# Kernel optimization log

Hardware: AMD Instinct MI355X
Metric: run time of the kernel (lower is better)

Reference implementation:

```python
import jax, jax.numpy as jnp
import numpy as np

EPS = 1e-5
NUM_HEADS = 8


def _conv(x, w, pad, dil=1, groups=1, b=None):
    y = jax.lax.conv_general_dilated(
        x, w, (1, 1), pad, rhs_dilation=(dil, dil),
        dimension_numbers=('NCHW', 'OIHW', 'NCHW'), feature_group_count=groups)
    if b is not None:
        y = y + b[None, :, None, None]
    return y


def _bn_relu(x, gamma, beta):
    # BatchNorm2d in training mode: batch statistics over (N,H,W) per channel
    mu = x.mean(axis=(0, 2, 3), keepdims=True)
    var = x.var(axis=(0, 2, 3), keepdims=True)
    y = (x - mu) / jnp.sqrt(var + EPS) * gamma[None, :, None, None] + beta[None, :, None, None]
    return jax.nn.relu(y)


def _ln(x, w, b):
    # WithBias LayerNorm over channel dim (to_3d makes C the last axis)
    mu = x.mean(axis=1, keepdims=True)
    var = x.var(axis=1, keepdims=True)
    return (x - mu) / jnp.sqrt(var + EPS) * w[None, :, None, None] + b[None, :, None, None]


def _l2n(t):
    # torch F.normalize: x / max(||x||_2, 1e-12)
    return t / jnp.maximum(jnp.linalg.norm(t, axis=-1, keepdims=True), 1e-12)


def _forward(x, ln_w, ln_b, wd1, gd1, bd1, wd2, gd2, bd2, wd3, gd3, bd3,
             w_out1, w1, b1, w2, b2, w3, b3, w4, b4, w5, b5, w6, b6, w_out2):
    B, C, H, W = x.shape
    head, ch = NUM_HEADS, C // NUM_HEADS
    x1 = _ln(x, ln_w, ln_b)
    # dilated dense-conv branch (DConv2d = conv -> BN -> ReLU), dilations [1,6,12]
    x11 = _bn_relu(_conv(x, wd1, ((0, 0), (0, 0))), gd1, bd1)
    x12 = _bn_relu(_conv(x, wd2, ((6, 6), (6, 6)), dil=6), gd2, bd2)
    x13 = _bn_relu(_conv(x, wd3, ((12, 12), (12, 12)), dil=12), gd3, bd3)
    out2 = _conv(x11 + x12 + x13, w_out1, ((0, 0), (0, 0))) + x
    # six depthwise conv branches, summed
    att = (_conv(x1, w1, ((0, 0), (2, 2)), groups=C, b=b1)
           + _conv(x1, w2, ((2, 2), (0, 0)), groups=C, b=b2)
           + _conv(x1, w3, ((0, 0), (0, 0)), groups=C, b=b3)
           + _conv(x1, w4, ((1, 1), (1, 1)), groups=C, b=b4)
           + _conv(x1, w5, ((0, 0), (3, 3)), groups=C, b=b5)
           + _conv(x1, w6, ((3, 3), (0, 0)), groups=C, b=b6))
    out1 = _conv(att, w_out2, ((0, 0), (0, 0)))

    def r_hwc(t):  # b (head c) h w -> b head h (w c)
        return t.reshape(B, head, ch, H, W).transpose(0, 1, 3, 4, 2).reshape(B, head, H, W * ch)

    def r_whc(t):  # b (head c) h w -> b head w (h c)
        return t.reshape(B, head, ch, H, W).transpose(0, 1, 4, 3, 2).reshape(B, head, W, H * ch)

    k1 = _l2n(r_hwc(out1))
    v1 = r_hwc(out1)
    k2 = _l2n(r_whc(out2))
    v2 = r_whc(out2)
    q2 = _l2n(r_whc(out1))
    q1 = _l2n(r_whc(out2))
    A1 = jax.nn.softmax(q1 @ jnp.swapaxes(k1, -2, -1), axis=-1)  # [B,head,W,H]
    out3 = A1 @ v1 + q1
    A2 = jax.nn.softmax(q2 @ jnp.swapaxes(k2, -2, -1), axis=-1)
    out4 = A2 @ v2 + q2
    # b head h (w c) -> b (head c) h w
    o3 = out3.reshape(B, head, H, W, ch).transpose(0, 1, 4, 2, 3).reshape(B, C, H, W)
    # b head w (h c) -> b (head c) h w
    o4 = out4.reshape(B, head, W, H, ch).transpose(0, 1, 4, 3, 2).reshape(B, C, H, W)
    return _conv(o3, w_out2, ((0, 0), (0, 0))) + _conv(o4, w_out2, ((0, 0), (0, 0))) + x


def setup_inputs() -> dict:
    key = jax.random.key(0)
    ks = jax.random.split(key, 16)
    B, C, H, W = 8, 128, 128, 128

    def rn(k, shape, s):
        return jax.random.normal(k, shape, jnp.float32) * s

    inp = {}
    inp['x'] = jax.random.normal(ks[0], (B, C, H, W), jnp.float32)
    inp['ln_w'] = jnp.ones((C,), jnp.float32)
    inp['ln_b'] = jnp.zeros((C,), jnp.float32)
    inp['wd1'] = rn(ks[1], (C, C, 1, 1), 0.1)
    inp['gd1'] = jnp.ones((C,), jnp.float32)
    inp['bd1'] = jnp.zeros((C,), jnp.float32)
    inp['wd2'] = rn(ks[2], (C, C, 3, 3), 0.04)
    inp['gd2'] = jnp.ones((C,), jnp.float32)
    inp['bd2'] = jnp.zeros((C,), jnp.float32)
    inp['wd3'] = rn(ks[3], (C, C, 3, 3), 0.04)
    inp['gd3'] = jnp.ones((C,), jnp.float32)
    inp['bd3'] = jnp.zeros((C,), jnp.float32)
    inp['w_out1'] = rn(ks[4], (C, C, 1, 1), 0.09)
    inp['w1'] = rn(ks[5], (C, 1, 1, 5), 0.3)
    inp['b1'] = jnp.zeros((C,), jnp.float32)
    inp['w2'] = rn(ks[6], (C, 1, 5, 1), 0.3)
    inp['b2'] = jnp.zeros((C,), jnp.float32)
    inp['w3'] = rn(ks[7], (C, 1, 1, 1), 0.5)
    inp['b3'] = jnp.zeros((C,), jnp.float32)
    inp['w4'] = rn(ks[8], (C, 1, 3, 3), 0.2)
    inp['b4'] = jnp.zeros((C,), jnp.float32)
    inp['w5'] = rn(ks[9], (C, 1, 1, 7), 0.25)
    inp['b5'] = jnp.zeros((C,), jnp.float32)
    inp['w6'] = rn(ks[10], (C, 1, 7, 1), 0.25)
    inp['b6'] = jnp.zeros((C,), jnp.float32)
    inp['w_out2'] = rn(ks[11], (C, C, 1, 1), 0.09)
    return inp


def reference(x, ln_w, ln_b, wd1, gd1, bd1, wd2, gd2, bd2, wd3, gd3, bd3,
              w_out1, w1, b1, w2, b2, w3, b3, w4, b4, w5, b5, w6, b6, w_out2):
    return _forward(x, ln_w, ln_b, wd1, gd1, bd1, wd2, gd2, bd2, wd3, gd3, bd3,
                    w_out1, w1, b1, w2, b2, w3, b3, w4, b4, w5, b5, w6, b6, w_out2)
```

## Files before the change

### kernel.cpp

```cpp
#include <hip/hip_runtime.h>

#define Bb 8
#define Cc 128
#define Hh 128
#define Ww 128
#define HW 16384
#define CHW (Cc*HW)
#define NHW (Bb*HW)
#define CH 16
#define EPS 1e-5f

typedef __attribute__((ext_vector_type(8))) short bf16x8;
typedef __attribute__((ext_vector_type(4))) float f32x4;

static __device__ __forceinline__ short f2b(float f) {
  unsigned u = __float_as_uint(f);
  unsigned lsb = (u >> 16) & 1;
  return (short)((u + 0x7fffu + lsb) >> 16);
}
static __device__ __forceinline__ float b2f(short s) {
  return __uint_as_float(((unsigned)(unsigned short)s) << 16);
}

__global__ __launch_bounds__(256) void k_ln(const float* __restrict__ x,
    const float* __restrict__ g, const float* __restrict__ be,
    float* __restrict__ y)
{
  int p = blockIdx.x*256 + threadIdx.x;
  int b = p >> 14, hw = p & 16383;
  const float* xp = x + (long)b*CHW + hw;
  float s = 0.f, q = 0.f;
  for (int c = 0; c < Cc; ++c) { float v = xp[c*HW]; s += v; q += v*v; }
  float mu = s * (1.f/Cc);
  float var = q * (1.f/Cc) - mu*mu;
  float rstd = rsqrtf(var + EPS);
  float* yp = y + (long)b*CHW + hw;
  for (int c = 0; c < Cc; ++c) {
    float v = xp[c*HW];
    yp[c*HW] = (v - mu) * rstd * g[c] + be[c];
  }
}

__global__ __launch_bounds__(256) void k_reorg3b(const float* __restrict__ Wt, short* __restrict__ out)
{
  int idx = blockIdx.x*256 + threadIdx.x;
  int tap = idx >> 14, r = idx & 16383;
  out[idx] = f2b(Wt[r*9 + tap]);
}

__global__ __launch_bounds__(256) void k_cast(const float* __restrict__ in, short* __restrict__ out)
{
  int i = blockIdx.x*256 + threadIdx.x;
  out[i] = f2b(in[i]);
}

__global__ __launch_bounds__(256) void k_zero(float* p, int n)
{
  int i = blockIdx.x*256 + threadIdx.x;
  if (i < n) p[i] = 0.f;
}

__global__ __launch_bounds__(256) void k_nhwc(const float* __restrict__ in, short* __restrict__ out)
{
  __shared__ float Ls[32][33];
  int bid = blockIdx.x;
  int hwt = bid & 511, c4 = (bid>>9)&3, b = bid>>11;
  int hw0 = hwt << 5, c0 = c4 << 5;
  int t = threadIdx.x;
  int hl = t & 31, cl = t >> 5;
  const float* p = in + (long)b*CHW + hw0;
  for (int r = cl; r < 32; r += 8)
    Ls[r][hl] = p[(long)(c0+r)*HW + hl];
  __syncthreads();
  short* q = out + ((long)b*HW + hw0)*Cc + c0;
  int ccl = t & 31, hl0 = t >> 5;
  for (int r = hl0; r < 32; r += 8)
    q[(long)r*Cc + ccl] = f2b(Ls[ccl][r]);
}

__global__ __launch_bounds__(256,2) void k_mconv(const short* __restrict__ X,
    const short* __restrict__ W, const float* __restrict__ res,
    float* __restrict__ Y, int k3, int dil)
{
  __shared__ short Ws[128*136];
  __shared__ short Xs[152*136];
  int b = blockIdx.x >> 7, h = blockIdx.x & 127;
  int t = threadIdx.x;
  int wave = t >> 6, lane = t & 63;
  int co0 = (wave >> 1) << 6, sp0 = (wave & 1) << 6;
  int lm = lane & 15, quad = lane >> 4;
  f32x4 acc[4][4];
  #pragma unroll
  for (int i = 0; i < 4; ++i)
    #pragma unroll
    for (int j = 0; j < 4; ++j) acc[i][j] = (f32x4){0.f,0.f,0.f,0.f};
  int half = k3 >> 1;

  {
    f32x4 z = {0.f,0.f,0.f,0.f};
    for (int i = t; i < 408; i += 256) {
      int r = i / 17, o = i - r*17;
      int row = r < 12 ? r : r + 128;
      *(f32x4*)(Xs + row*136 + o*8) = z;
    }
  }

  for (int kh = 0; kh < k3; ++kh) {
    int hs = h + (kh - half)*dil;
    if ((unsigned)hs >= (unsigned)Hh) continue;
    __syncthreads();
    {
      const short* xr = X + ((long)(b*Hh + hs)*Ww)*Cc;
      #pragma unroll
      for (int it = 0; it < 8; ++it) {
        int i = t + it*256;
        int row = i >> 4, off = (i & 15) << 3;
        *(f32x4*)(Xs + (12 + row)*136 + off) = *(const f32x4*)(xr + (long)row*Cc + off);
      }
    }
    for (int kw = 0; kw < k3; ++kw) {
      int dw = (kw - half)*dil;
      if (kw) __syncthreads();
      {
        const short* wt = W + (kh*k3 + kw)*16384;
        #pragma unroll
        for (int it = 0; it < 8; ++it) {
          int i = t + it*256;
          int row = i >> 4, off = (i & 15) << 3;
          *(f32x4*)(Ws + row*136 + off) = *(const f32x4*)(wt + (long)row*128 + off);
        }
      }
      __syncthreads();
      int xrow0 = 12 + dw + sp0;
      for (int kc = 0; kc < 4; ++kc) {
        int k0 = kc << 5;
        bf16x8 af[4], bfr[4];
        #pragma unroll
        for (int i = 0; i < 4; ++i)
          af[i] = *(const bf16x8*)(Ws + (co0 + i*16 + lm)*136 + k0 + quad*8);
        #pragma unroll
        for (int j = 0; j < 4; ++j)
          bfr[j] = *(const bf16x8*)(Xs + (xrow0 + j*16 + lm)*136 + k0 + quad*8);
        #pragma unroll
        for (int i = 0; i < 4; ++i)
          #pragma unroll
          for (int j = 0; j < 4; ++j)
            acc[i][j] = __builtin_amdgcn_mfma_f32_16x16x32_bf16(af[i], bfr[j], acc[i][j], 0, 0, 0);
      }
    }
  }
  #pragma unroll
  for (int i = 0; i < 4; ++i) {
    int co = co0 + i*16 + quad*4;
    #pragma unroll
    for (int j = 0; j < 4; ++j) {
      int wc = sp0 + j*16 + lm;
      long base = ((long)(b*Cc + co)*Hh + h)*Ww + wc;
      #pragma unroll
      for (int r = 0; r < 4; ++r) {
        float v = acc[i][j][r];
        long idx = base + (long)r*HW;
        if (res) v += res[idx];
        Y[idx] = v;
      }
    }
  }
}

__global__ __launch_bounds__(256,4) void k_mconv1(const short* __restrict__ X,
    const short* __restrict__ W, const float* __restrict__ res,
    float* __restrict__ Y)
{
  __shared__ short Ws[128*136];
  int b = blockIdx.x >> 7, h = blockIdx.x & 127;
  int t = threadIdx.x;
  int wave = t >> 6, lane = t & 63;
  int co0 = (wave >> 1) << 6, sp0 = (wave & 1) << 6;
  int lm = lane & 15, quad = lane >> 4;
  #pragma unroll
  for (int it = 0; it < 8; ++it) {
    int i = t + it*256;
    int row = i >> 4, off = (i & 15) << 3;
    *(f32x4*)(Ws + row*136 + off) = *(const f32x4*)(W + (long)row*128 + off);
  }
  f32x4 acc[4][4];
  #pragma unroll
  for (int i = 0; i < 4; ++i)
    #pragma unroll
    for (int j = 0; j < 4; ++j) acc[i][j] = (f32x4){0.f,0.f,0.f,0.f};
  const short* xr = X + ((long)(b*Hh + h)*Ww)*Cc;
  __syncthreads();
  #pragma unroll
  for (int kc = 0; kc < 4; ++kc) {
    int k0 = kc << 5;
    bf16x8 af[4], bfr[4];
    #pragma unroll
    for (int j = 0; j < 4; ++j)
      bfr[j] = *(const bf16x8*)(xr + (long)(sp0 + j*16 + lm)*Cc + k0 + quad*8);
    #pragma unroll
    for (int i = 0; i < 4; ++i)
      af[i] = *(const bf16x8*)(Ws + (co0 + i*16 + lm)*136 + k0 + quad*8);
    #pragma unroll
    for (int i = 0; i < 4; ++i)
      #pragma unroll
      for (int j = 0; j < 4; ++j)
        acc[i][j] = __builtin_amdgcn_mfma_f32_16x16x32_bf16(af[i], bfr[j], acc[i][j], 0, 0, 0);
  }
  #pragma unroll
  for (int i = 0; i < 4; ++i) {
    int co = co0 + i*16 + quad*4;
    #pragma unroll
    for (int j = 0; j < 4; ++j) {
      int wc = sp0 + j*16 + lm;
      long base = ((long)(b*Cc + co)*Hh + h)*Ww + wc;
      #pragma unroll
      for (int r = 0; r < 4; ++r) {
        float v = acc[i][j][r];
        long idx = base + (long)r*HW;
        if (res) v += res[idx];
        Y[idx] = v;
      }
    }
  }
}

__global__ __launch_bounds__(256) void k_bnstats(const float* __restrict__ y1,
    const float* __restrict__ y2, const float* __restrict__ y3,
    float* __restrict__ stats)
{
  __shared__ float red[512];
  int bid = blockIdx.x;
  int tsel = bid >> 10;
  int rem = bid & 1023;
  int c = rem >> 3, b = rem & 7;
  const float* y = tsel == 0 ? y1 : (tsel == 1 ? y2 : y3);
  const float* p = y + (long)(b*Cc + c)*HW;
  float s = 0.f, q = 0.f;
  for (int i = threadIdx.x; i < HW; i += 256) { float v = p[i]; s += v; q += v*v; }
  red[threadIdx.x] = s; red[256+threadIdx.x] = q;
  __syncthreads();
  for (int st = 128; st > 0; st >>= 1) {
    if (threadIdx.x < st) {
      red[threadIdx.x] += red[threadIdx.x+st];
      red[256+threadIdx.x] += red[256+threadIdx.x+st];
    }
    __syncthreads();
  }
  if (threadIdx.x == 0) {
    atomicAdd(&stats[tsel*256 + c], red[0]);
    atomicAdd(&stats[tsel*256 + 128 + c], red[256]);
  }
}

__global__ __launch_bounds__(256) void k_bnapply(const float* y1,
    const float* __restrict__ y2, const float* __restrict__ y3,
    const float* __restrict__ stats,
    const float* __restrict__ g1, const float* __restrict__ be1,
    const float* __restrict__ g2, const float* __restrict__ be2,
    const float* __restrict__ g3, const float* __restrict__ be3,
    float* out)
{
  int i4 = blockIdx.x*256 + threadIdx.x;
  int c = (i4 >> 12) & 127;
  const float inv = 1.f/(float)NHW;
  float mu1 = stats[c]*inv;       float v1 = stats[128+c]*inv - mu1*mu1;
  float mu2 = stats[256+c]*inv;   float v2 = stats[384+c]*inv - mu2*mu2;
  float mu3 = stats[512+c]*inv;   float v3 = stats[640+c]*inv - mu3*mu3;
  float s1 = rsqrtf(v1+EPS)*g1[c], s2 = rsqrtf(v2+EPS)*g2[c], s3 = rsqrtf(v3+EPS)*g3[c];
  float o1 = be1[c]-mu1*s1, o2 = be2[c]-mu2*s2, o3_ = be3[c]-mu3*s3;
  float4 a = ((const float4*)y1)[i4];
  float4 bq = ((const float4*)y2)[i4];
  float4 cq = ((const float4*)y3)[i4];
  float4 r;
  r.x = fmaxf(fmaf(a.x,s1,o1),0.f)+fmaxf(fmaf(bq.x,s2,o2),0.f)+fmaxf(fmaf(cq.x,s3,o3_),0.f);
  r.y = fmaxf(fmaf(a.y,s1,o1),0.f)+fmaxf(fmaf(bq.y,s2,o2),0.f)+fmaxf(fmaf(cq.y,s3,o3_),0.f);
  r.z = fmaxf(fmaf(a.z,s1,o1),0.f)+fmaxf(fmaf(bq.z,s2,o2),0.f)+fmaxf(fmaf(cq.z,s3,o3_),0.f);
  r.w = fmaxf(fmaf(a.w,s1,o1),0.f)+fmaxf(fmaf(bq.w,s2,o2),0.f)+fmaxf(fmaf(cq.w,s3,o3_),0.f);
  ((float4*)out)[i4] = r;
}

__global__ __launch_bounds__(256) void k_dw2(const float* __restrict__ X,
    const float* __restrict__ w1, const float* __restrict__ b1,
    const float* __restrict__ w2, const float* __restrict__ b2,
    const float* __restrict__ w3, const float* __restrict__ b3,
    const float* __restrict__ w4, const float* __restrict__ b4,
    const float* __restrict__ w5, const float* __restrict__ b5,
    const float* __restrict__ w6, const float* __restrict__ b6,
    float* __restrict__ Y)
{
  __shared__ float Ls[38][136];
  int bid = blockIdx.x;
  int tile = bid & 3, plane = bid >> 2;
  int c = plane & 127;
  int h0 = tile << 5;
  int t = threadIdx.x;

  float hcoef[7], vcoef[7], k9[9];
  #pragma unroll
  for (int d = 0; d < 7; ++d) { hcoef[d] = w5[c*7+d]; vcoef[d] = w6[c*7+d]; }
  #pragma unroll
  for (int d = 1; d < 6; ++d) { hcoef[d] += w1[c*5+d-1]; vcoef[d] += w2[c*5+d-1]; }
  hcoef[3] += w3[c];
  #pragma unroll
  for (int k = 0; k < 9; ++k) k9[k] = w4[c*9+k];
  float bias = b1[c]+b2[c]+b3[c]+b4[c]+b5[c]+b6[c];

  const float* xp = X + (long)plane*HW;

  f32x4* lz = (f32x4*)&Ls[0][0];
  for (int i = t; i < 1292; i += 256) lz[i] = (f32x4){0.f,0.f,0.f,0.f};
  __syncthreads();
  for (int i = t; i < 1216; i += 256) {
    int r = i >> 5, cg = (i & 31) << 2;
    int h = h0 - 3 + r;
    if ((unsigned)h < 128u)
      *(f32x4*)&Ls[r][4 + cg] = *(const f32x4*)(xp + h*128 + cg);
  }
  __syncthreads();

  int g = t & 31, rs = t >> 5;
  int w0 = g << 2;
  float* Yp = Y + (long)plane*HW;

  for (int ro = 0; ro < 4; ++ro) {
    int lr = rs + (ro << 3);
    int R = lr + 3;
    f32x4 a0 = *(const f32x4*)&Ls[R][w0];
    f32x4 a1 = *(const f32x4*)&Ls[R][w0+4];
    f32x4 a2 = *(const f32x4*)&Ls[R][w0+8];
    f32x4 u0 = *(const f32x4*)&Ls[R-1][w0];
    f32x4 u1 = *(const f32x4*)&Ls[R-1][w0+4];
    f32x4 u2 = *(const f32x4*)&Ls[R-1][w0+8];
    f32x4 d0 = *(const f32x4*)&Ls[R+1][w0];
    f32x4 d1 = *(const f32x4*)&Ls[R+1][w0+4];
    f32x4 d2 = *(const f32x4*)&Ls[R+1][w0+8];
    f32x4 v3u = *(const f32x4*)&Ls[R-3][w0+4];
    f32x4 v2u = *(const f32x4*)&Ls[R-2][w0+4];
    f32x4 v2d = *(const f32x4*)&Ls[R+2][w0+4];
    f32x4 v3d = *(const f32x4*)&Ls[R+3][w0+4];

    float cr[12], ur[12], dr[12];
    #pragma unroll
    for (int k = 0; k < 4; ++k) {
      cr[k] = a0[k]; cr[4+k] = a1[k]; cr[8+k] = a2[k];
      ur[k] = u0[k]; ur[4+k] = u1[k]; ur[8+k] = u2[k];
      dr[k] = d0[k]; dr[4+k] = d1[k]; dr[8+k] = d2[k];
    }

    f32x4 o;
    #pragma unroll
    for (int j = 0; j < 4; ++j) {
      float acc = bias;
      #pragma unroll
      for (int d = 0; d < 7; ++d) acc = fmaf(hcoef[d], cr[j+d+1], acc);
      acc = fmaf(vcoef[0], v3u[j], acc);
      acc = fmaf(vcoef[1], v2u[j], acc);
      acc = fmaf(vcoef[2], ur[j+4], acc);
      acc = fmaf(vcoef[3], cr[j+4], acc);
      acc = fmaf(vcoef[4], dr[j+4], acc);
      acc = fmaf(vcoef[5], v2d[j], acc);
      acc = fmaf(vcoef[6], v3d[j], acc);
      #pragma unroll
      for (int kw = 0; kw < 3; ++kw) {
        acc = fmaf(k9[kw],   ur[j+3+kw], acc);
        acc = fmaf(k9[3+kw], cr[j+3+kw], acc);
        acc = fmaf(k9[6+kw], dr[j+3+kw], acc);
      }
      o[j] = acc;
    }
    *(f32x4*)(Yp + (h0 + lr)*128 + w0) = o;
  }
}

__global__ __launch_bounds__(256) void k_normh(const float* __restrict__ out1, float* __restrict__ invn)
{
  __shared__ float red[256];
  int bid = blockIdx.x;
  int h = bid & 127; int bh = bid >> 7;
  int b = bh >> 3, hd = bh & 7;
  const float* p = out1 + ((long)(b*Cc + hd*CH)*Hh + h)*Ww;
  float s = 0.f;
  for (int e = threadIdx.x; e < 2048; e += 256) {
    int c = e >> 7, w = e & 127;
    float v = p[(long)c*HW + w];
    s += v*v;
  }
  red[threadIdx.x] = s; __syncthreads();
  for (int st = 128; st > 0; st >>= 1) {
    if (threadIdx.x < st) red[threadIdx.x] += red[threadIdx.x+st];
    __syncthreads();
  }
  if (threadIdx.x == 0) invn[bid] = 1.f/fmaxf(sqrtf(red[0]), 1e-12f);
}

__global__ __launch_bounds__(256) void k_normw_part(const float* __restrict__ out1,
    const float* __restrict__ out2, float* __restrict__ acc1, float* __restrict__ acc2)
{
  __shared__ float red[4][256];
  int bid = blockIdx.x;
  int c = bid & 15, bh = (bid >> 4) & 63, tsel = bid >> 10;
  int b = bh >> 3, hd = bh & 7;
  const float* p = (tsel ? out2 : out1) + (long)(b*Cc + hd*CH + c)*HW;
  int t = threadIdx.x;
  const float4* p4 = (const float4*)p;
  float s0 = 0.f, s1 = 0.f, s2 = 0.f, s3 = 0.f;
  for (int i = t; i < 4096; i += 256) {
    float4 v = p4[i];
    s0 += v.x*v.x; s1 += v.y*v.y; s2 += v.z*v.z; s3 += v.w*v.w;
  }
  red[0][t] = s0; red[1][t] = s1; red[2][t] = s2; red[3][t] = s3;
  __syncthreads();
  if (t < 128) {
    int j = t >> 5;
    int g = t & 31;
    float tot = 0.f;
    #pragma unroll
    for (int r = 0; r < 8; ++r) tot += red[j][g + r*32];
    atomicAdd((tsel ? acc2 : acc1) + bh*128 + g*4 + j, tot);
  }
}

__global__ __launch_bounds__(256) void k_finw(float* __restrict__ p)
{
  int i = blockIdx.x*256 + threadIdx.x;
  float v = p[i];
  p[i] = 1.f/fmaxf(sqrtf(v), 1e-12f);
}

__global__ __launch_bounds__(256) void k_t12(const float* __restrict__ out1,
    const float* __restrict__ out2, short* __restrict__ out1T, short* __restrict__ out2T)
{
  __shared__ float Ls[32][33];
  int bid = blockIdx.x;
  int wt = bid&3, ht=(bid>>2)&3, c=(bid>>4)&127, b=(bid>>11)&7, src=bid>>14;
  const float* in = (src ? out2 : out1) + (long)(b*128+c)*16384;
  short* outp = (src ? out2T : out1T) + ((long)(b*8 + (c>>4))*128)*2048 + (c&15)*128;
  int h0 = ht*32, w0 = wt*32;
  int t = threadIdx.x, li = t&31, r0 = t>>5;
  for (int r = r0; r < 32; r += 8)
    Ls[r][li] = in[(h0+r)*128 + w0 + li];
  __syncthreads();
  for (int r = r0; r < 32; r += 8)
    outp[(long)(w0+r)*2048 + h0 + li] = f2b(Ls[li][r]);
}

__global__ __launch_bounds__(256) void k_h12(const float* __restrict__ out1,
    const float* __restrict__ out2, short* __restrict__ out1H, short* __restrict__ out2H)
{
  int bid = blockIdx.x;
  int src = bid >> 13;
  long e = ((long)(bid & 8191)*256 + threadIdx.x) * 8;
  const float* p;
  short* dst;
  if (src) { p = out2 + e; dst = out2H + e; }
  else {
    int c = (int)((e>>7)&15), h = (int)((e>>11)&127), hd=(int)((e>>18)&7), b=(int)(e>>21);
    int pp = (int)(e & 127);
    p = out1 + (((long)(b*128 + hd*16 + c)*128 + h)*128 + pp);
    dst = out1H + e;
  }
  int4 o;
  o.x = ((int)(unsigned short)f2b(p[1])<<16) | (unsigned short)f2b(p[0]);
  o.y = ((int)(unsigned short)f2b(p[3])<<16) | (unsigned short)f2b(p[2]);
  o.z = ((int)(unsigned short)f2b(p[5])<<16) | (unsigned short)f2b(p[4]);
  o.w = ((int)(unsigned short)f2b(p[7])<<16) | (unsigned short)f2b(p[6]);
  *(int4*)dst = o;
}

__global__ __launch_bounds__(256) void k_attnS_m(
    const short* __restrict__ out1T, const short* __restrict__ out2T,
    const short* __restrict__ out1H,
    const float* __restrict__ invn1h, const float* __restrict__ invn1w,
    const float* __restrict__ invn2w,
    short* __restrict__ A1b, short* __restrict__ A2b)
{
  __shared__ short As[128*72];
  __shared__ short Bs[128*72];
  int bid = blockIdx.x;
  int type = bid >> 6, bh = bid & 63;
  const short* Aop = (type ? out1T : out2T) + (long)bh*262144;
  const short* Bop = (type ? out2T : out1H) + (long)bh*262144;
  const float* invrow = (type ? invn1w : invn2w) + bh*128;
  const float* invcol = (type ? invn2w : invn1h) + bh*128;
  short* Aout = (type ? A2b : A1b) + (long)bh*16384;
  int t = threadIdx.x;
  int wave = t >> 6, lane = t & 63, lm = lane & 15, quad = lane >> 4;
  int m0 = wave << 5;
  f32x4 acc[2][8];
  #pragma unroll
  for (int i = 0; i < 2; ++i)
    #pragma unroll
    for (int j = 0; j < 8; ++j) acc[i][j] = (f32x4){0.f,0.f,0.f,0.f};
  for (int kc = 0; kc < 32; ++kc) {
    int k0 = kc << 6;
    __syncthreads();
    #pragma unroll
    for (int i = 0; i < 4; ++i) {
      int e = t + i*256;
      int row = e >> 3, off = (e & 7) << 3;
      *(float4*)(As + row*72 + off) = *(const float4*)(Aop + (long)row*2048 + k0 + off);
      *(float4*)(Bs + row*72 + off) = *(const float4*)(Bop + (long)row*2048 + k0 + off);
    }
    __syncthreads();
    #pragma unroll
    for (int ks = 0; ks < 64; ks += 32) {
      bf16x8 af[2], bfj[8];
      #pragma unroll
      for (int i = 0; i < 2; ++i)
        af[i] = *(const bf16x8*)(As + (m0 + i*16 + lm)*72 + ks + quad*8);
      #pragma unroll
      for (int j = 0; j < 8; ++j)
        bfj[j] = *(const bf16x8*)(Bs + (j*16 + lm)*72 + ks + quad*8);
      #pragma unroll
      for (int i = 0; i < 2; ++i)
        #pragma unroll
        for (int j = 0; j < 8; ++j)
          acc[i][j] = __builtin_amdgcn_mfma_f32_16x16x32_bf16(af[i], bfj[j], acc[i][j], 0, 0, 0);
    }
  }
  float colv[8];
  #pragma unroll
  for (int j = 0; j < 8; ++j) colv[j] = invcol[j*16 + lm];
  #pragma unroll
  for (int i = 0; i < 2; ++i) {
    #pragma unroll
    for (int r = 0; r < 4; ++r) {
      int row = m0 + i*16 + quad*4 + r;
      float rs = invrow[row];
      float sv[8];
      float mx = -1e30f;
      #pragma unroll
      for (int j = 0; j < 8; ++j) {
        sv[j] = acc[i][j][r] * rs * colv[j];
        mx = fmaxf(mx, sv[j]);
      }
      mx = fmaxf(mx, __shfl_xor(mx, 1));
      mx = fmaxf(mx, __shfl_xor(mx, 2));
      mx = fmaxf(mx, __shfl_xor(mx, 4));
      mx = fmaxf(mx, __shfl_xor(mx, 8));
      float sum = 0.f;
      #pragma unroll
      for (int j = 0; j < 8; ++j) { sv[j] = __expf(sv[j] - mx); sum += sv[j]; }
      sum += __shfl_xor(sum, 1);
      sum += __shfl_xor(sum, 2);
      sum += __shfl_xor(sum, 4);
      sum += __shfl_xor(sum, 8);
      float inv = 1.f/sum;
      #pragma unroll
      for (int j = 0; j < 8; ++j)
        Aout[row*128 + j*16 + lm] = f2b(sv[j]*inv);
    }
  }
}

__global__ __launch_bounds__(256) void k_o34m(
    const short* __restrict__ A1b, const short* __restrict__ out1T,
    const short* __restrict__ out1H, const float* __restrict__ invn1w,
    const short* __restrict__ out2H, const short* __restrict__ A2b,
    float* __restrict__ o34, int mode)
{
  __shared__ short As[128*72];
  __shared__ short Bs[128*72];
  int bid = blockIdx.x;
  const short *Abase, *Bbase;
  long Astride, Bstride;
  float* O;
  const short* R = nullptr;
  const float* inw = nullptr;
  if (mode == 0) {
    int c = bid & 15, hd = (bid>>4)&7, b = bid>>7;
    int bh = b*8+hd;
    Abase = A1b + (long)bh*16384; Astride = 128;
    Bbase = out1T + (long)bh*262144 + c*128; Bstride = 2048;
    O = o34 + (long)(b*128 + hd*16 + c)*16384;
    R = out1H + (long)bh*262144 + c*128;
    inw = invn1w + bh*128;
  } else {
    int cf = bid & 127, b = bid >> 7;
    int bh = b*8 + (cf>>4);
    Abase = out2H + (long)(b*128+cf)*16384; Astride = 128;
    Bbase = A2b + (long)bh*16384; Bstride = 128;
    O = o34 + (long)(b*128+cf)*16384;
  }
  int t = threadIdx.x;
  int wave = t >> 6, lane = t & 63, lm = lane & 15, quad = lane >> 4;
  int m0 = (wave >> 1) << 6, n0 = (wave & 1) << 6;
  f32x4 acc[4][4];
  #pragma unroll
  for (int i = 0; i < 4; ++i)
    #pragma unroll
    for (int j = 0; j < 4; ++j) acc[i][j] = (f32x4){0.f,0.f,0.f,0.f};
  for (int kc = 0; kc < 2; ++kc) {
    int k0 = kc << 6;
    __syncthreads();
    #pragma unroll
    for (int i = 0; i < 4; ++i) {
      int e = t + i*256;
      int row = e >> 3, off = (e & 7) << 3;
      *(float4*)(As + row*72 + off) = *(const float4*)(Abase + (long)row*Astride + k0 + off);
      *(float4*)(Bs + row*72 + off) = *(const float4*)(Bbase + (long)row*Bstride + k0 + off);
    }
    __syncthreads();
    #pragma unroll
    for (int ks = 0; ks < 64; ks += 32) {
      bf16x8 af[4], bfj[4];
      #pragma unroll
      for (int i = 0; i < 4; ++i)
        af[i] = *(const bf16x8*)(As + (m0 + i*16 + lm)*72 + ks + quad*8);
      #pragma unroll
      for (int j = 0; j < 4; ++j)
        bfj[j] = *(const bf16x8*)(Bs + (n0 + j*16 + lm)*72 + ks + quad*8);
      #pragma unroll
      for (int i = 0; i < 4; ++i)
        #pragma unroll
        for (int j = 0; j < 4; ++j)
          acc[i][j] = __builtin_amdgcn_mfma_f32_16x16x32_bf16(af[i], bfj[j], acc[i][j], 0, 0, 0);
    }
  }
  if (mode == 0) {
    float inwv[4];
    #pragma unroll
    for (int j = 0; j < 4; ++j) inwv[j] = inw[n0 + j*16 + lm];
    #pragma unroll
    for (int i = 0; i < 4; ++i) {
      #pragma unroll
      for (int r = 0; r < 4; ++r) {
        int row = m0 + i*16 + quad*4 + r;
        #pragma unroll
        for (int j = 0; j < 4; ++j) {
          int col = n0 + j*16 + lm;
          float rv = b2f(R[(long)row*2048 + col]);
          O[row*128 + col] = acc[i][j][r] + rv * inwv[j];
        }
      }
    }
  } else {
    #pragma unroll
    for (int i = 0; i < 4; ++i) {
      #pragma unroll
      for (int r = 0; r < 4; ++r) {
        int row = m0 + i*16 + quad*4 + r;
        #pragma unroll
        for (int j = 0; j < 4; ++j) {
          int col = n0 + j*16 + lm;
          O[row*128 + col] += acc[i][j][r];
        }
      }
    }
  }
}

__global__ __launch_bounds__(256) void k_tadd(const float* __restrict__ out2,
    const float* __restrict__ invn2w, float* o34)
{
  __shared__ float Ls[32][33];
  int bid = blockIdx.x;
  int wi = bid & 3, hi = (bid>>2)&3, cc = (bid>>4)&127, b = bid>>11;
  int h0 = hi*32, w0 = wi*32;
  int hd = cc >> 4;
  int t = threadIdx.x;
  int li = t & 31, r0 = t >> 5;
  const float* p = out2 + (long)(b*Cc+cc)*HW;
  for (int r = r0; r < 32; r += 8)
    Ls[r][li] = p[(w0+r)*128 + h0 + li];
  __syncthreads();
  float* q = o34 + (long)(b*Cc+cc)*HW;
  for (int r = r0; r < 32; r += 8) {
    float iv = invn2w[(((b<<3)+hd)<<7) + h0 + r];
    q[(h0+r)*128 + w0 + li] += Ls[li][r] * iv;
  }
}

extern "C" void kernel_launch(void* const* d_in, const int* in_sizes, int n_in,
                              void* d_out, int out_size, void* d_ws, size_t ws_size,
                              hipStream_t stream)
{
  const float* x    = (const float*)d_in[0];
  const float* ln_w = (const float*)d_in[1];
  const float* ln_b = (const float*)d_in[2];
  const float* wd1  = (const float*)d_in[3];
  const float* gd1  = (const float*)d_in[4];
  const float* bd1  = (const float*)d_in[5];
  const float* wd2  = (const float*)d_in[6];
  const float* gd2  = (const float*)d_in[7];
  const float* bd2  = (const float*)d_in[8];
  const float* wd3  = (const float*)d_in[9];
  const float* gd3  = (const float*)d_in[10];
  const float* bd3  = (const float*)d_in[11];
  const float* w_out1 = (const float*)d_in[12];
  const float* w1 = (const float*)d_in[13]; const float* b1 = (const float*)d_in[14];
  const float* w2 = (const float*)d_in[15]; const float* b2 = (const float*)d_in[16];
  const float* w3 = (const float*)d_in[17]; const float* b3 = (const float*)d_in[18];
  const float* w4 = (const float*)d_in[19]; const float* b4 = (const float*)d_in[20];
  const float* w5 = (const float*)d_in[21]; const float* b5 = (const float*)d_in[22];
  const float* w6 = (const float*)d_in[23]; const float* b6 = (const float*)d_in[24];
  const float* w_out2 = (const float*)d_in[25];
  float* out = (float*)d_out;

  const long SLAB = 16777216L;
  float* buf0 = (float*)d_ws;
  float* buf1 = buf0 + SLAB;
  float* buf2 = buf1 + SLAB;
  float* dbuf = out;
  float* stats = buf2 + SLAB;
  float* invn1h = stats + 768;
  float* invn1w = invn1h + 8192;
  float* invn2w = invn1w + 8192;
  short* wb2  = (short*)(invn2w + 8192);
  short* wb3  = wb2 + 147456;
  short* wb1  = wb3 + 147456;
  short* wbo1 = wb1 + 16384;
  short* wbo2 = wbo1 + 16384;
  short* A1b  = wbo2 + 16384;
  short* A2b  = A1b + 1048576;

  short* xb = (short*)buf0;
  short* sb = (short*)dbuf;
  short* ab = (short*)buf1;
  short* out1T = (short*)dbuf;
  short* out2T = out1T + 16777216;
  short* out1H = (short*)buf1;
  short* out2H = out1H + 16777216;
  short* ob = (short*)buf1;

  k_zero<<<3, 256, 0, stream>>>(stats, 768);
  k_zero<<<64, 256, 0, stream>>>(invn1w, 16384);
  k_reorg3b<<<576, 256, 0, stream>>>(wd2, wb2);
  k_reorg3b<<<576, 256, 0, stream>>>(wd3, wb3);
  k_cast<<<64, 256, 0, stream>>>(wd1, wb1);
  k_cast<<<64, 256, 0, stream>>>(w_out1, wbo1);
  k_cast<<<64, 256, 0, stream>>>(w_out2, wbo2);

  k_nhwc<<<16384, 256, 0, stream>>>(x, xb);
  k_mconv1<<<1024, 256, 0, stream>>>(xb, wb1, nullptr, buf1);
  k_mconv<<<1024, 256, 0, stream>>>(xb, wb2, nullptr, buf2, 3, 6);
  k_mconv<<<1024, 256, 0, stream>>>(xb, wb3, nullptr, dbuf, 3, 12);
  k_bnstats<<<3072, 256, 0, stream>>>(buf1, buf2, dbuf, stats);
  k_bnapply<<<16384, 256, 0, stream>>>(buf1, buf2, dbuf, stats,
                                       gd1, bd1, gd2, bd2, gd3, bd3, buf1);
  k_ln<<<512, 256, 0, stream>>>(x, ln_w, ln_b, buf0);
  k_nhwc<<<16384, 256, 0, stream>>>(buf1, sb);
  k_mconv1<<<1024, 256, 0, stream>>>(sb, wbo1, x, buf2);
  k_dw2<<<4096, 256, 0, stream>>>(buf0, w1,b1,w2,b2,w3,b3,w4,b4,w5,b5,w6,b6, dbuf);
  k_nhwc<<<16384, 256, 0, stream>>>(dbuf, ab);
  k_mconv1<<<1024, 256, 0, stream>>>(ab, wbo2, nullptr, buf0);
  k_normh<<<8192, 256, 0, stream>>>(buf0, invn1h);
  k_normw_part<<<2048, 256, 0, stream>>>(buf0, buf2, invn1w, invn2w);
  k_finw<<<64, 256, 0, stream>>>(invn1w);
  k_t12<<<32768, 256, 0, stream>>>(buf0, buf2, out1T, out2T);
  k_h12<<<16384, 256, 0, stream>>>(buf0, buf2, out1H, out2H);
  k_attnS_m<<<128, 256, 0, stream>>>(out1T, out2T, out1H,
                                     invn1h, invn1w, invn2w, A1b, A2b);
  k_o34m<<<1024, 256, 0, stream>>>(A1b, out1T, out1H, invn1w,
                                   out2H, A2b, buf0, 0);
  k_o34m<<<1024, 256, 0, stream>>>(A1b, out1T, out1H, invn1w,
                                   out2H, A2b, buf0, 1);
  k_tadd<<<16384, 256, 0, stream>>>(buf2, invn2w, buf0);
  k_nhwc<<<16384, 256, 0, stream>>>(buf0, ob);
  k_mconv1<<<1024, 256, 0, stream>>>(ob, wbo2, x, out);
}
```

Baseline: 898.8 us.

## Keep dilated conv outputs in NHWC, fuse BN apply with bf16 NHWC cast

The three dilated-branch convolutions now write NHWC float outputs with vector stores. BN stats are reduced along the channel-contiguous layout, and a small finalize kernel precomputes scale and offset. BN-apply then writes bf16 NHWC directly, which removes one k_nhwc transpose pass over the full activation. The NCHW epilogue of mconv1 now stages each tile through LDS so it can use vector stores with a vectorized residual add, at the cost of extra LDS traffic and a barrier.

```diff
diff --git a/kernel.cpp b/kernel.cpp
--- a/kernel.cpp
+++ b/kernel.cpp
@@ -79,8 +79,7 @@
 }
 
 __global__ __launch_bounds__(256,2) void k_mconv(const short* __restrict__ X,
-    const short* __restrict__ W, const float* __restrict__ res,
-    float* __restrict__ Y, int k3, int dil)
+    const short* __restrict__ W, float* __restrict__ Y, int k3, int dil)
 {
   __shared__ short Ws[128*136];
   __shared__ short Xs[152*136];
@@ -149,27 +148,21 @@
       }
     }
   }
+  float* yb = Y + ((long)(b*Hh + h)*Ww)*Cc;
   #pragma unroll
   for (int i = 0; i < 4; ++i) {
     int co = co0 + i*16 + quad*4;
     #pragma unroll
     for (int j = 0; j < 4; ++j) {
       int wc = sp0 + j*16 + lm;
-      long base = ((long)(b*Cc + co)*Hh + h)*Ww + wc;
-      #pragma unroll
-      for (int r = 0; r < 4; ++r) {
-        float v = acc[i][j][r];
-        long idx = base + (long)r*HW;
-        if (res) v += res[idx];
-        Y[idx] = v;
-      }
+      *(f32x4*)(yb + (long)wc*Cc + co) = acc[i][j];
     }
   }
 }
 
 __global__ __launch_bounds__(256,4) void k_mconv1(const short* __restrict__ X,
     const short* __restrict__ W, const float* __restrict__ res,
-    float* __restrict__ Y)
+    float* __restrict__ Y, int nhwc)
 {
   __shared__ short Ws[128*136];
   int b = blockIdx.x >> 7, h = blockIdx.x & 127;
@@ -206,19 +199,34 @@
       for (int j = 0; j < 4; ++j)
         acc[i][j] = __builtin_amdgcn_mfma_f32_16x16x32_bf16(af[i], bfr[j], acc[i][j], 0, 0, 0);
   }
-  #pragma unroll
-  for (int i = 0; i < 4; ++i) {
-    int co = co0 + i*16 + quad*4;
-    #pragma unroll
-    for (int j = 0; j < 4; ++j) {
-      int wc = sp0 + j*16 + lm;
-      long base = ((long)(b*Cc + co)*Hh + h)*Ww + wc;
-      #pragma unroll
-      for (int r = 0; r < 4; ++r) {
-        float v = acc[i][j][r];
-        long idx = base + (long)r*HW;
-        if (res) v += res[idx];
-        Y[idx] = v;
+  if (nhwc) {
+    float* yb = Y + ((long)(b*Hh + h)*Ww)*Cc;
+    #pragma unroll
+    for (int i = 0; i < 4; ++i) {
+      int co = co0 + i*16 + quad*4;
+      #pragma unroll
+      for (int j = 0; j < 4; ++j) {
+        int wc = sp0 + j*16 + lm;
+        *(f32x4*)(yb + (long)wc*Cc + co) = acc[i][j];
+      }
+    }
+  } else {
+    __syncthreads();
+    float* scr = (float*)Ws + wave*320;
+    int co_l = lane >> 2, wq = (lane & 3) << 2;
+    #pragma unroll
+    for (int i = 0; i < 4; ++i) {
+      #pragma unroll
+      for (int j = 0; j < 4; ++j) {
+        #pragma unroll
+        for (int r = 0; r < 4; ++r)
+          scr[(quad*4 + r)*20 + lm] = acc[i][j][r];
+        f32x4 vv = *(f32x4*)(scr + co_l*20 + wq);
+        int co = co0 + i*16 + co_l;
+        int wc = sp0 + j*16 + wq;
+        long idx = ((long)(b*Cc + co)*Hh + h)*Ww + wc;
+        if (res) vv += *(const f32x4*)(res + idx);
+        *(f32x4*)(Y + idx) = vv;
       }
     }
   }
@@ -228,55 +236,83 @@
     const float* __restrict__ y2, const float* __restrict__ y3,
     float* __restrict__ stats)
 {
-  __shared__ float red[512];
-  int bid = blockIdx.x;
-  int tsel = bid >> 10;
-  int rem = bid & 1023;
-  int c = rem >> 3, b = rem & 7;
+  __shared__ f32x4 Ls[8][32], Lq[8][32];
+  int bid = blockIdx.x;
+  int pt = bid & 31, b = (bid >> 5) & 7, tsel = bid >> 8;
   const float* y = tsel == 0 ? y1 : (tsel == 1 ? y2 : y3);
-  const float* p = y + (long)(b*Cc + c)*HW;
-  float s = 0.f, q = 0.f;
-  for (int i = threadIdx.x; i < HW; i += 256) { float v = p[i]; s += v; q += v*v; }
-  red[threadIdx.x] = s; red[256+threadIdx.x] = q;
+  const f32x4* p4 = (const f32x4*)(y + ((long)b*HW + pt*512)*Cc);
+  int t = threadIdx.x;
+  int cg = t & 31, pr = t >> 5;
+  f32x4 s = {0.f,0.f,0.f,0.f}, q = {0.f,0.f,0.f,0.f};
+  for (int k = 0; k < 64; ++k) {
+    f32x4 v = p4[(long)(pr + k*8)*32 + cg];
+    s += v; q += v*v;
+  }
+  Ls[pr][cg] = s; Lq[pr][cg] = q;
   __syncthreads();
-  for (int st = 128; st > 0; st >>= 1) {
-    if (threadIdx.x < st) {
-      red[threadIdx.x] += red[threadIdx.x+st];
-      red[256+threadIdx.x] += red[256+threadIdx.x+st];
-    }
-    __syncthreads();
-  }
-  if (threadIdx.x == 0) {
-    atomicAdd(&stats[tsel*256 + c], red[0]);
-    atomicAdd(&stats[tsel*256 + 128 + c], red[256]);
-  }
-}
-
-__global__ __launch_bounds__(256) void k_bnapply(const float* y1,
-    const float* __restrict__ y2, const float* __restrict__ y3,
-    const float* __restrict__ stats,
+  if (t < 32) {
+    f32x4 ts = {0.f,0.f,0.f,0.f}, tq = {0.f,0.f,0.f,0.f};
+    #pragma unroll
+    for (int r = 0; r < 8; ++r) { ts += Ls[r][t]; tq += Lq[r][t]; }
+    #pragma unroll
+    for (int e = 0; e < 4; ++e) {
+      atomicAdd(&stats[tsel*256 + t*4 + e], ts[e]);
+      atomicAdd(&stats[tsel*256 + 128 + t*4 + e], tq[e]);
+    }
+  }
+}
+
+__global__ __launch_bounds__(128) void k_bnfin(const float* __restrict__ stats,
     const float* __restrict__ g1, const float* __restrict__ be1,
     const float* __restrict__ g2, const float* __restrict__ be2,
     const float* __restrict__ g3, const float* __restrict__ be3,
-    float* out)
-{
-  int i4 = blockIdx.x*256 + threadIdx.x;
-  int c = (i4 >> 12) & 127;
+    float* __restrict__ so)
+{
+  int c = threadIdx.x;
   const float inv = 1.f/(float)NHW;
-  float mu1 = stats[c]*inv;       float v1 = stats[128+c]*inv - mu1*mu1;
-  float mu2 = stats[256+c]*inv;   float v2 = stats[384+c]*inv - mu2*mu2;
-  float mu3 = stats[512+c]*inv;   float v3 = stats[640+c]*inv - mu3*mu3;
-  float s1 = rsqrtf(v1+EPS)*g1[c], s2 = rsqrtf(v2+EPS)*g2[c], s3 = rsqrtf(v3+EPS)*g3[c];
-  float o1 = be1[c]-mu1*s1, o2 = be2[c]-mu2*s2, o3_ = be3[c]-mu3*s3;
-  float4 a = ((const float4*)y1)[i4];
-  float4 bq = ((const float4*)y2)[i4];
-  float4 cq = ((const float4*)y3)[i4];
-  float4 r;
-  r.x = fmaxf(fmaf(a.x,s1,o1),0.f)+fmaxf(fmaf(bq.x,s2,o2),0.f)+fmaxf(fmaf(cq.x,s3,o3_),0.f);
-  r.y = fmaxf(fmaf(a.y,s1,o1),0.f)+fmaxf(fmaf(bq.y,s2,o2),0.f)+fmaxf(fmaf(cq.y,s3,o3_),0.f);
-  r.z = fmaxf(fmaf(a.z,s1,o1),0.f)+fmaxf(fmaf(bq.z,s2,o2),0.f)+fmaxf(fmaf(cq.z,s3,o3_),0.f);
-  r.w = fmaxf(fmaf(a.w,s1,o1),0.f)+fmaxf(fmaf(bq.w,s2,o2),0.f)+fmaxf(fmaf(cq.w,s3,o3_),0.f);
-  ((float4*)out)[i4] = r;
+  const float* gs[3] = {g1, g2, g3};
+  const float* bs[3] = {be1, be2, be3};
+  #pragma unroll
+  for (int tsel = 0; tsel < 3; ++tsel) {
+    float mu = stats[tsel*256 + c]*inv;
+    float var = stats[tsel*256 + 128 + c]*inv - mu*mu;
+    float s = rsqrtf(var + EPS)*gs[tsel][c];
+    so[tsel*256 + c] = s;
+    so[tsel*256 + 128 + c] = bs[tsel][c] - mu*s;
+  }
+}
+
+__global__ __launch_bounds__(256) void k_bnapply(const float* __restrict__ y1,
+    const float* __restrict__ y2, const float* __restrict__ y3,
+    const float* __restrict__ so, short* __restrict__ sb)
+{
+  long e = ((long)blockIdx.x*256 + threadIdx.x) * 8;
+  int c = (int)(e & 127);
+  f32x4 s1a = *(const f32x4*)(so + c),        s1b = *(const f32x4*)(so + c + 4);
+  f32x4 o1a = *(const f32x4*)(so + 128 + c),  o1b = *(const f32x4*)(so + 132 + c);
+  f32x4 s2a = *(const f32x4*)(so + 256 + c),  s2b = *(const f32x4*)(so + 260 + c);
+  f32x4 o2a = *(const f32x4*)(so + 384 + c),  o2b = *(const f32x4*)(so + 388 + c);
+  f32x4 s3a = *(const f32x4*)(so + 512 + c),  s3b = *(const f32x4*)(so + 516 + c);
+  f32x4 o3a = *(const f32x4*)(so + 640 + c),  o3b = *(const f32x4*)(so + 644 + c);
+  f32x4 v1a = *(const f32x4*)(y1 + e), v1b = *(const f32x4*)(y1 + e + 4);
+  f32x4 v2a = *(const f32x4*)(y2 + e), v2b = *(const f32x4*)(y2 + e + 4);
+  f32x4 v3a = *(const f32x4*)(y3 + e), v3b = *(const f32x4*)(y3 + e + 4);
+  float r[8];
+  #pragma unroll
+  for (int k = 0; k < 4; ++k) {
+    r[k] = fmaxf(fmaf(v1a[k], s1a[k], o1a[k]), 0.f)
+         + fmaxf(fmaf(v2a[k], s2a[k], o2a[k]), 0.f)
+         + fmaxf(fmaf(v3a[k], s3a[k], o3a[k]), 0.f);
+    r[4+k] = fmaxf(fmaf(v1b[k], s1b[k], o1b[k]), 0.f)
+           + fmaxf(fmaf(v2b[k], s2b[k], o2b[k]), 0.f)
+           + fmaxf(fmaf(v3b[k], s3b[k], o3b[k]), 0.f);
+  }
+  int4 o;
+  o.x = ((int)(unsigned short)f2b(r[1])<<16) | (unsigned short)f2b(r[0]);
+  o.y = ((int)(unsigned short)f2b(r[3])<<16) | (unsigned short)f2b(r[2]);
+  o.z = ((int)(unsigned short)f2b(r[5])<<16) | (unsigned short)f2b(r[4]);
+  o.w = ((int)(unsigned short)f2b(r[7])<<16) | (unsigned short)f2b(r[6]);
+  *(int4*)(sb + e) = o;
 }
 
 __global__ __launch_bounds__(256) void k_dw2(const float* __restrict__ X,
@@ -713,9 +749,10 @@
   short* wbo2 = wbo1 + 16384;
   short* A1b  = wbo2 + 16384;
   short* A2b  = A1b + 1048576;
+  float* bnso = (float*)(A2b + 1048576);
 
   short* xb = (short*)buf0;
-  short* sb = (short*)dbuf;
+  short* sb = (short*)buf0;
   short* ab = (short*)buf1;
   short* out1T = (short*)dbuf;
   short* out2T = out1T + 16777216;
@@ -732,18 +769,17 @@
   k_cast<<<64, 256, 0, stream>>>(w_out2, wbo2);
 
   k_nhwc<<<16384, 256, 0, stream>>>(x, xb);
-  k_mconv1<<<1024, 256, 0, stream>>>(xb, wb1, nullptr, buf1);
-  k_mconv<<<1024, 256, 0, stream>>>(xb, wb2, nullptr, buf2, 3, 6);
-  k_mconv<<<1024, 256, 0, stream>>>(xb, wb3, nullptr, dbuf, 3, 12);
-  k_bnstats<<<3072, 256, 0, stream>>>(buf1, buf2, dbuf, stats);
-  k_bnapply<<<16384, 256, 0, stream>>>(buf1, buf2, dbuf, stats,
-                                       gd1, bd1, gd2, bd2, gd3, bd3, buf1);
+  k_mconv1<<<1024, 256, 0, stream>>>(xb, wb1, nullptr, buf1, 1);
+  k_mconv<<<1024, 256, 0, stream>>>(xb, wb2, buf2, 3, 6);
+  k_mconv<<<1024, 256, 0, stream>>>(xb, wb3, dbuf, 3, 12);
+  k_bnstats<<<768, 256, 0, stream>>>(buf1, buf2, dbuf, stats);
+  k_bnfin<<<1, 128, 0, stream>>>(stats, gd1, bd1, gd2, bd2, gd3, bd3, bnso);
+  k_bnapply<<<8192, 256, 0, stream>>>(buf1, buf2, dbuf, bnso, sb);
+  k_mconv1<<<1024, 256, 0, stream>>>(sb, wbo1, x, buf2, 0);
   k_ln<<<512, 256, 0, stream>>>(x, ln_w, ln_b, buf0);
-  k_nhwc<<<16384, 256, 0, stream>>>(buf1, sb);
-  k_mconv1<<<1024, 256, 0, stream>>>(sb, wbo1, x, buf2);
   k_dw2<<<4096, 256, 0, stream>>>(buf0, w1,b1,w2,b2,w3,b3,w4,b4,w5,b5,w6,b6, dbuf);
   k_nhwc<<<16384, 256, 0, stream>>>(dbuf, ab);
-  k_mconv1<<<1024, 256, 0, stream>>>(ab, wbo2, nullptr, buf0);
+  k_mconv1<<<1024, 256, 0, stream>>>(ab, wbo2, nullptr, buf0, 0);
   k_normh<<<8192, 256, 0, stream>>>(buf0, invn1h);
   k_normw_part<<<2048, 256, 0, stream>>>(buf0, buf2, invn1w, invn2w);
   k_finw<<<64, 256, 0, stream>>>(invn1w);
@@ -757,5 +793,5 @@
                                    out2H, A2b, buf0, 1);
   k_tadd<<<16384, 256, 0, stream>>>(buf2, invn2w, buf0);
   k_nhwc<<<16384, 256, 0, stream>>>(buf0, ob);
-  k_mconv1<<<1024, 256, 0, stream>>>(ob, wbo2, x, out);
-}
+  k_mconv1<<<1024, 256, 0, stream>>>(ob, wbo2, x, out, 0);
+}
```

After: 840.1 us. 1.07x faster.
